# Optimization experiments

Measured on AMD Instinct MI355X. Metric: run time of the kernel, lower is better.

Reference implementation:

```python
import jax, jax.numpy as jnp
import numpy as np

B, T = 256, 64
ACT, EMB = 6, 1024
S, D = 32, 32          # stoch, discrete
SF = S * D             # flattened stochastic state (1024)
DET, HID = 600, 600


def _st_sample(logit, g):
    """Gumbel-max categorical sample with straight-through gradient.
    logit, g: [B, S, D]. Returns one-hot sample [B, S, D]."""
    idx = jnp.argmax(logit + g, axis=-1)
    onehot = jax.nn.one_hot(idx, logit.shape[-1], dtype=logit.dtype)
    probs = jax.nn.softmax(logit, axis=-1)
    return onehot + probs - jax.lax.stop_gradient(probs)


def setup_inputs() -> dict:
    key = jax.random.key(0)
    ks = jax.random.split(key, 20)
    p = lambda k, shp: (jax.random.normal(k, shp, dtype=jnp.float32) * 0.02)
    inp = {
        "action": jax.random.normal(ks[0], (B, T, ACT), dtype=jnp.float32),
        "embed": jax.random.normal(ks[1], (B, T, EMB), dtype=jnp.float32),
        "noise_img": jax.random.gumbel(ks[2], (B, T, S, D), dtype=jnp.float32),
        "noise_obs": jax.random.gumbel(ks[3], (B, T, S, D), dtype=jnp.float32),
        # img1: Dense(hidden, elu) on concat([stoch, action])
        "W_img1": p(ks[4], (SF + ACT, HID)), "b_img1": jnp.zeros((HID,), jnp.float32),
        # keras GRUCell (reset_after=True): gate order z, r, h; two biases
        "Wx": p(ks[5], (HID, 3 * DET)), "Wh": p(ks[6], (DET, 3 * DET)),
        "b_in": jnp.zeros((3 * DET,), jnp.float32), "b_rec": jnp.zeros((3 * DET,), jnp.float32),
        # img2: Dense(hidden, elu); img5: Dense(stoch*discrete)
        "W_img2": p(ks[7], (DET, HID)), "b_img2": jnp.zeros((HID,), jnp.float32),
        "W_img5": p(ks[8], (HID, SF)), "b_img5": jnp.zeros((SF,), jnp.float32),
        # obs1: Dense(hidden, elu) on concat([deter, embed]); obs3: Dense(stoch*discrete)
        "W_obs1": p(ks[9], (DET + EMB, HID)), "b_obs1": jnp.zeros((HID,), jnp.float32),
        "W_obs3": p(ks[10], (HID, SF)), "b_obs3": jnp.zeros((SF,), jnp.float32),
    }
    return inp


def reference(action, embed, noise_img, noise_obs,
              W_img1, b_img1, Wx, Wh, b_in, b_rec,
              W_img2, b_img2, W_img5, b_img5,
              W_obs1, b_obs1, W_obs3, b_obs3):
    # initial state: zeros (RSSM.initial)
    stoch0 = jnp.zeros((B, SF), jnp.float32)
    deter0 = jnp.zeros((B, DET), jnp.float32)

    def step(carry, inp):
        stoch, deter = carry                       # [B,SF], [B,DET]
        a, e, g_img, g_obs = inp
        # ---- img_step (prior) ----
        x = jax.nn.elu(jnp.concatenate([stoch, a], -1) @ W_img1 + b_img1)  # [B,HID]
        gx = x @ Wx + b_in                         # [B,3*DET]
        gh = deter @ Wh + b_rec
        xz, xr, xh = jnp.split(gx, 3, -1)
        hz, hr, hh = jnp.split(gh, 3, -1)
        z = jax.nn.sigmoid(xz + hz)
        r = jax.nn.sigmoid(xr + hr)
        cand = jnp.tanh(xh + r * hh)
        deter_n = z * deter + (1.0 - z) * cand     # [B,DET]
        y = jax.nn.elu(deter_n @ W_img2 + b_img2)
        logit_prior = (y @ W_img5 + b_img5).reshape(B, S, D)
        stoch_prior = _st_sample(logit_prior, g_img).reshape(B, SF)
        # ---- obs_step (post) ----
        o = jax.nn.elu(jnp.concatenate([deter_n, e], -1) @ W_obs1 + b_obs1)
        logit_post = (o @ W_obs3 + b_obs3).reshape(B, S, D)
        stoch_post = _st_sample(logit_post, g_obs).reshape(B, SF)
        out = (logit_post.reshape(B, SF), stoch_post, deter_n,
               logit_prior.reshape(B, SF), stoch_prior)
        return (stoch_post, deter_n), out

    xs = (jnp.swapaxes(action, 0, 1), jnp.swapaxes(embed, 0, 1),
          jnp.swapaxes(noise_img, 0, 1), jnp.swapaxes(noise_obs, 0, 1))
    _, outs = jax.lax.scan(step, (stoch0, deter0), xs)
    # outs: each [T,B,*] -> [B,T,*]; concat post_logit|post_stoch|deter|prior_logit|prior_stoch
    out = jnp.concatenate([jnp.swapaxes(o, 0, 1) for o in outs], axis=-1)  # [B,T,4*SF+DET]
    return out
```

## Files before the change

### kernel.cpp

```cpp
#include <hip/hip_runtime.h>
#include <math.h>

namespace {

constexpr int B = 256, T = 64, ACTN = 6, EMB = 1024;
constexpr int S = 32, DD = 32, SFN = 1024;
constexpr int DET = 600, HID = 600;
constexpr int OUTF = 4 * SFN + DET;

__device__ __forceinline__ float elu1(float x) { return x > 0.f ? x : expm1f(x); }
__device__ __forceinline__ float sigm(float x) { return 1.f / (1.f + expf(-x)); }

__global__ void kWB(const float* __restrict__ Wx, const float* __restrict__ Wh,
                    float* __restrict__ WBm) {
    int k = blockIdx.x;
    const float* src = (k < 600) ? (Wx + (size_t)k * 1800) : (Wh + (size_t)(k - 600) * 1800);
    for (int j = threadIdx.x; j < 600; j += blockDim.x) {
        size_t o = ((size_t)j * 1200 + k) * 3;
        WBm[o + 0] = src[j];
        WBm[o + 1] = src[600 + j];
        WBm[o + 2] = src[1200 + j];
    }
}

__global__ void kWC(const float* __restrict__ W2, const float* __restrict__ Wo1,
                    float* __restrict__ WCm) {
    int k = blockIdx.x;
    for (int j = threadIdx.x; j < 1200; j += blockDim.x) {
        float v = (j < 600) ? W2[(size_t)k * 600 + j] : Wo1[(size_t)k * 600 + (j - 600)];
        WCm[(size_t)j * 600 + k] = v;
    }
}

__global__ void kWD(const float* __restrict__ W5, const float* __restrict__ Wo3,
                    float* __restrict__ WDm) {
    int k = blockIdx.x;
    for (int j = threadIdx.x; j < 2048; j += blockDim.x) {
        float v = (j < 1024) ? W5[(size_t)k * 1024 + j] : Wo3[(size_t)k * 1024 + (j - 1024)];
        WDm[(size_t)j * 600 + k] = v;
    }
}

__global__ __launch_bounds__(512) void kPemb(const float* __restrict__ embed,
                                             const float* __restrict__ Wo1,
                                             const float* __restrict__ bo1,
                                             float* __restrict__ embPre) {
    int bid = blockIdx.x;
    int jg = bid % 10;
    int r = bid / 10;
    int bg = r & 3;
    int t = r >> 2;
    int tid = threadIdx.x;
    int lane = tid & 63;
    int wid = __builtin_amdgcn_readfirstlane(tid >> 6);
    int b0 = bg * 64;
    int j0 = jg * 64 + wid * 8;
    bool active = (j0 < 600);
    __shared__ float tile[64 * 129];
    float acc[8] = {0, 0, 0, 0, 0, 0, 0, 0};
    for (int kc = 0; kc < EMB; kc += 128) {
        __syncthreads();
        for (int ii = tid; ii < 64 * 128; ii += 512) {
            int i = ii >> 7, k = ii & 127;
            tile[i * 129 + k] = embed[((size_t)(b0 + i) * T + t) * EMB + kc + k];
        }
        __syncthreads();
        if (active) {
            const float* wbase = Wo1 + (size_t)(600 + kc) * 600 + j0;
#pragma unroll 4
            for (int k = 0; k < 128; ++k) {
                float v = tile[lane * 129 + k];
                float4 wa = *(const float4*)(wbase + (size_t)k * 600);
                float4 wb = *(const float4*)(wbase + (size_t)k * 600 + 4);
                acc[0] += v * wa.x; acc[1] += v * wa.y; acc[2] += v * wa.z; acc[3] += v * wa.w;
                acc[4] += v * wb.x; acc[5] += v * wb.y; acc[6] += v * wb.z; acc[7] += v * wb.w;
            }
        }
    }
    if (active) {
#pragma unroll
        for (int c = 0; c < 8; ++c)
            embPre[((size_t)t * 600 + j0 + c) * B + b0 + lane] = acc[c] + bo1[j0 + c];
    }
}

__global__ __launch_bounds__(256) void kA(const float* __restrict__ act,
                                          const float* __restrict__ W1,
                                          const float* __restrict__ b1,
                                          const int* __restrict__ idxB,
                                          float* __restrict__ xT, int t, int first) {
    int b = blockIdx.x, tid = threadIdx.x;
    __shared__ float sa[ACTN];
    __shared__ int si[S];
    if (tid < ACTN) sa[tid] = act[((size_t)b * T + t) * ACTN + tid];
    if (!first && tid < S) si[tid] = idxB[b * S + tid];
    __syncthreads();
    for (int h = tid; h < HID; h += 256) {
        float a = b1[h];
#pragma unroll
        for (int k = 0; k < ACTN; ++k) a += sa[k] * W1[(size_t)(SFN + k) * HID + h];
        if (!first) {
#pragma unroll 8
            for (int s = 0; s < S; ++s) a += W1[(size_t)(s * DD + si[s]) * HID + h];
        }
        xT[(size_t)h * B + b] = elu1(a);
    }
}

__global__ __launch_bounds__(512) void kB(const float* __restrict__ xT,
                                          const float* __restrict__ dPrev,
                                          const float* __restrict__ WBm,
                                          const float* __restrict__ b_in,
                                          const float* __restrict__ b_rec,
                                          float* __restrict__ dNext,
                                          float* __restrict__ out, int t) {
    int tid = threadIdx.x, lane = tid & 63;
    int wid = __builtin_amdgcn_readfirstlane(tid >> 6);
    int rg = blockIdx.x & 3, jg = blockIdx.x >> 2;
    int j = jg * 8 + wid;
    int b = rg * 64 + lane;
    const float* w = WBm + (size_t)j * 3600;
    float az = 0, ar = 0, ax = 0, ah = 0;
#pragma unroll 2
    for (int k = 0; k < 600; k += 4) {
        float4 wa = *(const float4*)(w + 3 * k);
        float4 wb = *(const float4*)(w + 3 * k + 4);
        float4 wc = *(const float4*)(w + 3 * k + 8);
        float x0 = xT[(size_t)(k + 0) * B + b];
        float x1 = xT[(size_t)(k + 1) * B + b];
        float x2 = xT[(size_t)(k + 2) * B + b];
        float x3 = xT[(size_t)(k + 3) * B + b];
        az += x0 * wa.x + x1 * wa.w + x2 * wb.z + x3 * wc.y;
        ar += x0 * wa.y + x1 * wb.x + x2 * wb.w + x3 * wc.z;
        ax += x0 * wa.z + x1 * wb.y + x2 * wc.x + x3 * wc.w;
    }
    const float* w2 = w + 1800;
#pragma unroll 2
    for (int k = 0; k < 600; k += 4) {
        float4 wa = *(const float4*)(w2 + 3 * k);
        float4 wb = *(const float4*)(w2 + 3 * k + 4);
        float4 wc = *(const float4*)(w2 + 3 * k + 8);
        float x0 = dPrev[(size_t)(k + 0) * B + b];
        float x1 = dPrev[(size_t)(k + 1) * B + b];
        float x2 = dPrev[(size_t)(k + 2) * B + b];
        float x3 = dPrev[(size_t)(k + 3) * B + b];
        az += x0 * wa.x + x1 * wa.w + x2 * wb.z + x3 * wc.y;
        ar += x0 * wa.y + x1 * wb.x + x2 * wb.w + x3 * wc.z;
        ah += x0 * wa.z + x1 * wb.y + x2 * wc.x + x3 * wc.w;
    }
    float dp = dPrev[(size_t)j * B + b];
    float z = sigm(az + b_in[j] + b_rec[j]);
    float rr = sigm(ar + b_in[600 + j] + b_rec[600 + j]);
    float cand = tanhf(ax + b_in[1200 + j] + rr * (ah + b_rec[1200 + j]));
    float dn = z * dp + (1.f - z) * cand;
    dNext[(size_t)j * B + b] = dn;
    out[((size_t)b * T + t) * OUTF + 2 * SFN + j] = dn;
}

__global__ __launch_bounds__(512) void kC(const float* __restrict__ dT,
                                          const float* __restrict__ WCm,
                                          const float* __restrict__ b2,
                                          const float* __restrict__ embPre,
                                          float* __restrict__ yoT, int t) {
    int tid = threadIdx.x, lane = tid & 63;
    int wid = __builtin_amdgcn_readfirstlane(tid >> 6);
    int rg = blockIdx.x & 3, jg = blockIdx.x >> 2;
    int j0 = jg * 16 + wid * 2;
    int b = rg * 64 + lane;
    const float* w0 = WCm + (size_t)j0 * 600;
    const float* w1 = w0 + 600;
    float a0 = 0, a1 = 0;
#pragma unroll 2
    for (int k = 0; k < 600; k += 4) {
        float4 p = *(const float4*)(w0 + k);
        float4 q = *(const float4*)(w1 + k);
        float v0 = dT[(size_t)(k + 0) * B + b];
        float v1 = dT[(size_t)(k + 1) * B + b];
        float v2 = dT[(size_t)(k + 2) * B + b];
        float v3 = dT[(size_t)(k + 3) * B + b];
        a0 += v0 * p.x + v1 * p.y + v2 * p.z + v3 * p.w;
        a1 += v0 * q.x + v1 * q.y + v2 * q.z + v3 * q.w;
    }
    if (j0 < 600) {
        yoT[(size_t)j0 * B + b] = elu1(a0 + b2[j0]);
        yoT[(size_t)(j0 + 1) * B + b] = elu1(a1 + b2[j0 + 1]);
    } else {
        int je = j0 - 600;
        yoT[(size_t)j0 * B + b] = elu1(a0 + embPre[((size_t)t * 600 + je) * B + b]);
        yoT[(size_t)(j0 + 1) * B + b] = elu1(a1 + embPre[((size_t)t * 600 + je + 1) * B + b]);
    }
}

__global__ __launch_bounds__(512) void kD(const float* __restrict__ yoT,
                                          const float* __restrict__ WDm,
                                          const float* __restrict__ b5,
                                          const float* __restrict__ bo3,
                                          const float* __restrict__ gImg,
                                          const float* __restrict__ gObs,
                                          float* __restrict__ out,
                                          int* __restrict__ idxB, int t) {
    int tid = threadIdx.x, lane = tid & 63;
    int wid = __builtin_amdgcn_readfirstlane(tid >> 6);
    int rg = blockIdx.x & 3, sg = blockIdx.x >> 2;
    int post = (sg >= 32) ? 1 : 0;
    int s = post ? sg - 32 : sg;
    int b = rg * 64 + lane;
    int dloc = wid * 4;
    int jglob = post * SFN + s * DD + dloc;
    const float* src = yoT + (post ? (size_t)600 * B : 0);
    const float* w0 = WDm + (size_t)jglob * 600;
    const float* w1 = w0 + 600;
    const float* w2 = w0 + 1200;
    const float* w3 = w0 + 1800;
    float a0 = 0, a1 = 0, a2 = 0, a3 = 0;
#pragma unroll 2
    for (int k = 0; k < 600; k += 4) {
        float4 p0 = *(const float4*)(w0 + k);
        float4 p1 = *(const float4*)(w1 + k);
        float4 p2 = *(const float4*)(w2 + k);
        float4 p3 = *(const float4*)(w3 + k);
        float v0 = src[(size_t)(k + 0) * B + b];
        float v1 = src[(size_t)(k + 1) * B + b];
        float v2 = src[(size_t)(k + 2) * B + b];
        float v3 = src[(size_t)(k + 3) * B + b];
        a0 += v0 * p0.x + v1 * p0.y + v2 * p0.z + v3 * p0.w;
        a1 += v0 * p1.x + v1 * p1.y + v2 * p1.z + v3 * p1.w;
        a2 += v0 * p2.x + v1 * p2.y + v2 * p2.z + v3 * p2.w;
        a3 += v0 * p3.x + v1 * p3.y + v2 * p3.z + v3 * p3.w;
    }
    const float* bias = post ? (bo3 + s * DD) : (b5 + s * DD);
    const float* g = (post ? gObs : gImg) + ((size_t)b * T + t) * SFN + s * DD;
    size_t obase = ((size_t)b * T + t) * OUTF;
    size_t lbase = obase + (post ? 0 : (2 * SFN + DET)) + s * DD;
    float vals[4];
    float accs[4] = {a0, a1, a2, a3};
#pragma unroll
    for (int c = 0; c < 4; ++c) {
        float lg = accs[c] + bias[dloc + c];
        out[lbase + dloc + c] = lg;
        vals[c] = lg + g[dloc + c];
    }
    float bm = vals[0];
    int bi = dloc;
#pragma unroll
    for (int c = 1; c < 4; ++c)
        if (vals[c] > bm) { bm = vals[c]; bi = dloc + c; }
    __shared__ float sm[8 * 64];
    __shared__ int sx[8 * 64];
    sm[wid * 64 + lane] = bm;
    sx[wid * 64 + lane] = bi;
    __syncthreads();
    float best = sm[lane];
    int bd = sx[lane];
#pragma unroll
    for (int w = 1; w < 8; ++w) {
        float v = sm[w * 64 + lane];
        if (v > best) { best = v; bd = sx[w * 64 + lane]; }
    }
    size_t sbase = obase + (post ? SFN : (3 * SFN + DET)) + s * DD;
#pragma unroll
    for (int c = 0; c < 4; ++c)
        out[sbase + dloc + c] = (dloc + c == bd) ? 1.f : 0.f;
    if (post && wid == 0) idxB[b * S + s] = bd;
}

}

extern "C" void kernel_launch(void* const* d_in, const int* in_sizes, int n_in,
                              void* d_out, int out_size, void* d_ws, size_t ws_size,
                              hipStream_t stream) {
    const float* action = (const float*)d_in[0];
    const float* embed  = (const float*)d_in[1];
    const float* gImg   = (const float*)d_in[2];
    const float* gObs   = (const float*)d_in[3];
    const float* W1     = (const float*)d_in[4];
    const float* b1     = (const float*)d_in[5];
    const float* Wx     = (const float*)d_in[6];
    const float* Wh     = (const float*)d_in[7];
    const float* b_in   = (const float*)d_in[8];
    const float* b_rec  = (const float*)d_in[9];
    const float* W2     = (const float*)d_in[10];
    const float* b2     = (const float*)d_in[11];
    const float* W5     = (const float*)d_in[12];
    const float* b5     = (const float*)d_in[13];
    const float* Wo1    = (const float*)d_in[14];
    const float* bo1    = (const float*)d_in[15];
    const float* Wo3    = (const float*)d_in[16];
    const float* bo3    = (const float*)d_in[17];
    float* out = (float*)d_out;

    float* ws = (float*)d_ws;
    float* WBm    = ws;
    float* WCm    = WBm + 2160000;
    float* WDm    = WCm + 720000;
    float* embPre = WDm + 1228800;
    float* xT     = embPre + 9830400;
    float* dA     = xT + 153600;
    float* dB     = dA + 153600;
    float* yoT    = dB + 153600;
    int*   idxB   = (int*)(yoT + 307200);

    hipMemsetAsync(dA, 0, 153600 * sizeof(float), stream);
    kWB<<<1200, 256, 0, stream>>>(Wx, Wh, WBm);
    kWC<<<600, 256, 0, stream>>>(W2, Wo1, WCm);
    kWD<<<600, 256, 0, stream>>>(W5, Wo3, WDm);
    kPemb<<<2560, 512, 0, stream>>>(embed, Wo1, bo1, embPre);

    for (int t = 0; t < T; ++t) {
        float* dP = (t & 1) ? dB : dA;
        float* dN = (t & 1) ? dA : dB;
        kA<<<256, 256, 0, stream>>>(action, W1, b1, idxB, xT, t, t == 0 ? 1 : 0);
        kB<<<300, 512, 0, stream>>>(xT, dP, WBm, b_in, b_rec, dN, out, t);
        kC<<<300, 512, 0, stream>>>(dN, WCm, b2, embPre, yoT, t);
        kD<<<256, 512, 0, stream>>>(yoT, WDm, b5, bo3, gImg, gObs, out, idxB, t);
    }
}
```

Baseline: 10.57 ms.

## Retile recurrent GEMV kernels so each wavefront covers 16 batches × 4 outputs

The GRU, hidden-dense and logit kernels are remapped so a 64-lane wavefront covers 16 batch rows by 4 output columns instead of 64 batch rows by one column. Weight rows are split per gate into separate planes. The categorical argmax in kD is now done with cross-lane shuffles instead of shared memory and a barrier. The goal is more weight reuse per load, lane-varying weight addresses, and more blocks for kC and kD. The cost is partly uncoalesced weight loads across the four column groups and different register pressure.

```diff
diff --git a/kernel.cpp b/kernel.cpp
--- a/kernel.cpp
+++ b/kernel.cpp
@@ -12,14 +12,12 @@
 __device__ __forceinline__ float sigm(float x) { return 1.f / (1.f + expf(-x)); }
 
 __global__ void kWB(const float* __restrict__ Wx, const float* __restrict__ Wh,
-                    float* __restrict__ WBm) {
+                    float* __restrict__ WBg) {
     int k = blockIdx.x;
     const float* src = (k < 600) ? (Wx + (size_t)k * 1800) : (Wh + (size_t)(k - 600) * 1800);
-    for (int j = threadIdx.x; j < 600; j += blockDim.x) {
-        size_t o = ((size_t)j * 1200 + k) * 3;
-        WBm[o + 0] = src[j];
-        WBm[o + 1] = src[600 + j];
-        WBm[o + 2] = src[1200 + j];
+    for (int i = threadIdx.x; i < 1800; i += blockDim.x) {
+        int g = i / 600, j = i % 600;
+        WBg[(size_t)g * 720000 + (size_t)j * 1200 + k] = src[i];
     }
 }
 
@@ -107,91 +105,118 @@
     }
 }
 
-__global__ __launch_bounds__(512) void kB(const float* __restrict__ xT,
+__global__ __launch_bounds__(256) void kB(const float* __restrict__ xT,
                                           const float* __restrict__ dPrev,
-                                          const float* __restrict__ WBm,
+                                          const float* __restrict__ WBg,
                                           const float* __restrict__ b_in,
                                           const float* __restrict__ b_rec,
                                           float* __restrict__ dNext,
                                           float* __restrict__ out, int t) {
-    int tid = threadIdx.x, lane = tid & 63;
-    int wid = __builtin_amdgcn_readfirstlane(tid >> 6);
-    int rg = blockIdx.x & 3, jg = blockIdx.x >> 2;
-    int j = jg * 8 + wid;
-    int b = rg * 64 + lane;
-    const float* w = WBm + (size_t)j * 3600;
-    float az = 0, ar = 0, ax = 0, ah = 0;
+    int tid = threadIdx.x, lane = tid & 63, wv = tid >> 6;
+    int bl = lane & 15, jl = lane >> 4;
+    int jg = blockIdx.x >> 2;
+    int bg = (blockIdx.x & 3) * 4 + wv;
+    int b = bg * 16 + bl;
+    int j0 = jg * 8 + jl;
+    const float* wz = WBg + (size_t)j0 * 1200;
+    const float* wr = wz + 720000;
+    const float* wc = wz + 1440000;
+    const float* xa = xT + b;
+    const float* da = dPrev + b;
+    float az0 = 0, ar0 = 0, ax0 = 0, ah0 = 0;
+    float az1 = 0, ar1 = 0, ax1 = 0, ah1 = 0;
 #pragma unroll 2
     for (int k = 0; k < 600; k += 4) {
-        float4 wa = *(const float4*)(w + 3 * k);
-        float4 wb = *(const float4*)(w + 3 * k + 4);
-        float4 wc = *(const float4*)(w + 3 * k + 8);
-        float x0 = xT[(size_t)(k + 0) * B + b];
-        float x1 = xT[(size_t)(k + 1) * B + b];
-        float x2 = xT[(size_t)(k + 2) * B + b];
-        float x3 = xT[(size_t)(k + 3) * B + b];
-        az += x0 * wa.x + x1 * wa.w + x2 * wb.z + x3 * wc.y;
-        ar += x0 * wa.y + x1 * wb.x + x2 * wb.w + x3 * wc.z;
-        ax += x0 * wa.z + x1 * wb.y + x2 * wc.x + x3 * wc.w;
-    }
-    const float* w2 = w + 1800;
+        float x0 = xa[(size_t)(k + 0) * B];
+        float x1 = xa[(size_t)(k + 1) * B];
+        float x2 = xa[(size_t)(k + 2) * B];
+        float x3 = xa[(size_t)(k + 3) * B];
+        float4 z0 = *(const float4*)(wz + k), z1 = *(const float4*)(wz + 4800 + k);
+        float4 r0 = *(const float4*)(wr + k), r1 = *(const float4*)(wr + 4800 + k);
+        float4 c0 = *(const float4*)(wc + k), c1 = *(const float4*)(wc + 4800 + k);
+        az0 += x0 * z0.x + x1 * z0.y + x2 * z0.z + x3 * z0.w;
+        az1 += x0 * z1.x + x1 * z1.y + x2 * z1.z + x3 * z1.w;
+        ar0 += x0 * r0.x + x1 * r0.y + x2 * r0.z + x3 * r0.w;
+        ar1 += x0 * r1.x + x1 * r1.y + x2 * r1.z + x3 * r1.w;
+        ax0 += x0 * c0.x + x1 * c0.y + x2 * c0.z + x3 * c0.w;
+        ax1 += x0 * c1.x + x1 * c1.y + x2 * c1.z + x3 * c1.w;
+    }
 #pragma unroll 2
     for (int k = 0; k < 600; k += 4) {
-        float4 wa = *(const float4*)(w2 + 3 * k);
-        float4 wb = *(const float4*)(w2 + 3 * k + 4);
-        float4 wc = *(const float4*)(w2 + 3 * k + 8);
-        float x0 = dPrev[(size_t)(k + 0) * B + b];
-        float x1 = dPrev[(size_t)(k + 1) * B + b];
-        float x2 = dPrev[(size_t)(k + 2) * B + b];
-        float x3 = dPrev[(size_t)(k + 3) * B + b];
-        az += x0 * wa.x + x1 * wa.w + x2 * wb.z + x3 * wc.y;
-        ar += x0 * wa.y + x1 * wb.x + x2 * wb.w + x3 * wc.z;
-        ah += x0 * wa.z + x1 * wb.y + x2 * wc.x + x3 * wc.w;
-    }
-    float dp = dPrev[(size_t)j * B + b];
-    float z = sigm(az + b_in[j] + b_rec[j]);
-    float rr = sigm(ar + b_in[600 + j] + b_rec[600 + j]);
-    float cand = tanhf(ax + b_in[1200 + j] + rr * (ah + b_rec[1200 + j]));
-    float dn = z * dp + (1.f - z) * cand;
-    dNext[(size_t)j * B + b] = dn;
-    out[((size_t)b * T + t) * OUTF + 2 * SFN + j] = dn;
-}
-
-__global__ __launch_bounds__(512) void kC(const float* __restrict__ dT,
+        float x0 = da[(size_t)(k + 0) * B];
+        float x1 = da[(size_t)(k + 1) * B];
+        float x2 = da[(size_t)(k + 2) * B];
+        float x3 = da[(size_t)(k + 3) * B];
+        float4 z0 = *(const float4*)(wz + 600 + k), z1 = *(const float4*)(wz + 5400 + k);
+        float4 r0 = *(const float4*)(wr + 600 + k), r1 = *(const float4*)(wr + 5400 + k);
+        float4 c0 = *(const float4*)(wc + 600 + k), c1 = *(const float4*)(wc + 5400 + k);
+        az0 += x0 * z0.x + x1 * z0.y + x2 * z0.z + x3 * z0.w;
+        az1 += x0 * z1.x + x1 * z1.y + x2 * z1.z + x3 * z1.w;
+        ar0 += x0 * r0.x + x1 * r0.y + x2 * r0.z + x3 * r0.w;
+        ar1 += x0 * r1.x + x1 * r1.y + x2 * r1.z + x3 * r1.w;
+        ah0 += x0 * c0.x + x1 * c0.y + x2 * c0.z + x3 * c0.w;
+        ah1 += x0 * c1.x + x1 * c1.y + x2 * c1.z + x3 * c1.w;
+    }
+    size_t ob = ((size_t)b * T + t) * OUTF + 2 * SFN;
+    {
+        int j = j0;
+        float dp = dPrev[(size_t)j * B + b];
+        float z = sigm(az0 + b_in[j] + b_rec[j]);
+        float rr = sigm(ar0 + b_in[600 + j] + b_rec[600 + j]);
+        float cd = tanhf(ax0 + b_in[1200 + j] + rr * (ah0 + b_rec[1200 + j]));
+        float dn = z * dp + (1.f - z) * cd;
+        dNext[(size_t)j * B + b] = dn;
+        out[ob + j] = dn;
+    }
+    {
+        int j = j0 + 4;
+        float dp = dPrev[(size_t)j * B + b];
+        float z = sigm(az1 + b_in[j] + b_rec[j]);
+        float rr = sigm(ar1 + b_in[600 + j] + b_rec[600 + j]);
+        float cd = tanhf(ax1 + b_in[1200 + j] + rr * (ah1 + b_rec[1200 + j]));
+        float dn = z * dp + (1.f - z) * cd;
+        dNext[(size_t)j * B + b] = dn;
+        out[ob + j] = dn;
+    }
+}
+
+__global__ __launch_bounds__(256) void kC(const float* __restrict__ dT,
                                           const float* __restrict__ WCm,
                                           const float* __restrict__ b2,
                                           const float* __restrict__ embPre,
                                           float* __restrict__ yoT, int t) {
-    int tid = threadIdx.x, lane = tid & 63;
-    int wid = __builtin_amdgcn_readfirstlane(tid >> 6);
-    int rg = blockIdx.x & 3, jg = blockIdx.x >> 2;
-    int j0 = jg * 16 + wid * 2;
-    int b = rg * 64 + lane;
+    int tid = threadIdx.x, lane = tid & 63, wv = tid >> 6;
+    int bl = lane & 15, jl = lane >> 4;
+    int jg = blockIdx.x >> 2;
+    int bg = (blockIdx.x & 3) * 4 + wv;
+    int b = bg * 16 + bl;
+    int j0 = jg * 8 + jl;
     const float* w0 = WCm + (size_t)j0 * 600;
-    const float* w1 = w0 + 600;
+    const float* w1 = w0 + 2400;
+    const float* da = dT + b;
     float a0 = 0, a1 = 0;
 #pragma unroll 2
     for (int k = 0; k < 600; k += 4) {
+        float x0 = da[(size_t)(k + 0) * B];
+        float x1 = da[(size_t)(k + 1) * B];
+        float x2 = da[(size_t)(k + 2) * B];
+        float x3 = da[(size_t)(k + 3) * B];
         float4 p = *(const float4*)(w0 + k);
         float4 q = *(const float4*)(w1 + k);
-        float v0 = dT[(size_t)(k + 0) * B + b];
-        float v1 = dT[(size_t)(k + 1) * B + b];
-        float v2 = dT[(size_t)(k + 2) * B + b];
-        float v3 = dT[(size_t)(k + 3) * B + b];
-        a0 += v0 * p.x + v1 * p.y + v2 * p.z + v3 * p.w;
-        a1 += v0 * q.x + v1 * q.y + v2 * q.z + v3 * q.w;
-    }
-    if (j0 < 600) {
-        yoT[(size_t)j0 * B + b] = elu1(a0 + b2[j0]);
-        yoT[(size_t)(j0 + 1) * B + b] = elu1(a1 + b2[j0 + 1]);
-    } else {
-        int je = j0 - 600;
-        yoT[(size_t)j0 * B + b] = elu1(a0 + embPre[((size_t)t * 600 + je) * B + b]);
-        yoT[(size_t)(j0 + 1) * B + b] = elu1(a1 + embPre[((size_t)t * 600 + je + 1) * B + b]);
-    }
-}
-
-__global__ __launch_bounds__(512) void kD(const float* __restrict__ yoT,
+        a0 += x0 * p.x + x1 * p.y + x2 * p.z + x3 * p.w;
+        a1 += x0 * q.x + x1 * q.y + x2 * q.z + x3 * q.w;
+    }
+#pragma unroll
+    for (int ja = 0; ja < 2; ++ja) {
+        int j = j0 + 4 * ja;
+        float a = ja ? a1 : a0;
+        float v = (j < 600) ? elu1(a + b2[j])
+                            : elu1(a + embPre[((size_t)t * 600 + (j - 600)) * B + b]);
+        yoT[(size_t)j * B + b] = v;
+    }
+}
+
+__global__ __launch_bounds__(128) void kD(const float* __restrict__ yoT,
                                           const float* __restrict__ WDm,
                                           const float* __restrict__ b5,
                                           const float* __restrict__ bo3,
@@ -199,69 +224,51 @@
                                           const float* __restrict__ gObs,
                                           float* __restrict__ out,
                                           int* __restrict__ idxB, int t) {
-    int tid = threadIdx.x, lane = tid & 63;
-    int wid = __builtin_amdgcn_readfirstlane(tid >> 6);
-    int rg = blockIdx.x & 3, sg = blockIdx.x >> 2;
+    int tid = threadIdx.x, lane = tid & 63, wv = tid >> 6;
+    int bl = lane & 15, jl = lane >> 4;
+    int sg = blockIdx.x >> 3;
+    int bg = (blockIdx.x & 7) * 2 + wv;
     int post = (sg >= 32) ? 1 : 0;
     int s = post ? sg - 32 : sg;
-    int b = rg * 64 + lane;
-    int dloc = wid * 4;
-    int jglob = post * SFN + s * DD + dloc;
-    const float* src = yoT + (post ? (size_t)600 * B : 0);
-    const float* w0 = WDm + (size_t)jglob * 600;
-    const float* w1 = w0 + 600;
-    const float* w2 = w0 + 1200;
-    const float* w3 = w0 + 1800;
-    float a0 = 0, a1 = 0, a2 = 0, a3 = 0;
+    int b = bg * 16 + bl;
+    const float* src = yoT + (post ? (size_t)600 * B : 0) + b;
+    const float* w = WDm + ((size_t)(post * SFN) + s * DD + jl) * 600;
+    float acc[8] = {0, 0, 0, 0, 0, 0, 0, 0};
 #pragma unroll 2
     for (int k = 0; k < 600; k += 4) {
-        float4 p0 = *(const float4*)(w0 + k);
-        float4 p1 = *(const float4*)(w1 + k);
-        float4 p2 = *(const float4*)(w2 + k);
-        float4 p3 = *(const float4*)(w3 + k);
-        float v0 = src[(size_t)(k + 0) * B + b];
-        float v1 = src[(size_t)(k + 1) * B + b];
-        float v2 = src[(size_t)(k + 2) * B + b];
-        float v3 = src[(size_t)(k + 3) * B + b];
-        a0 += v0 * p0.x + v1 * p0.y + v2 * p0.z + v3 * p0.w;
-        a1 += v0 * p1.x + v1 * p1.y + v2 * p1.z + v3 * p1.w;
-        a2 += v0 * p2.x + v1 * p2.y + v2 * p2.z + v3 * p2.w;
-        a3 += v0 * p3.x + v1 * p3.y + v2 * p3.z + v3 * p3.w;
-    }
-    const float* bias = post ? (bo3 + s * DD) : (b5 + s * DD);
-    const float* g = (post ? gObs : gImg) + ((size_t)b * T + t) * SFN + s * DD;
+        float x0 = src[(size_t)(k + 0) * B];
+        float x1 = src[(size_t)(k + 1) * B];
+        float x2 = src[(size_t)(k + 2) * B];
+        float x3 = src[(size_t)(k + 3) * B];
+#pragma unroll
+        for (int ja = 0; ja < 8; ++ja) {
+            float4 p = *(const float4*)(w + (size_t)ja * 2400 + k);
+            acc[ja] += x0 * p.x + x1 * p.y + x2 * p.z + x3 * p.w;
+        }
+    }
+    const float* bias = (post ? bo3 : b5) + s * DD + jl;
+    const float* g = (post ? gObs : gImg) + ((size_t)b * T + t) * SFN + s * DD + jl;
     size_t obase = ((size_t)b * T + t) * OUTF;
-    size_t lbase = obase + (post ? 0 : (2 * SFN + DET)) + s * DD;
-    float vals[4];
-    float accs[4] = {a0, a1, a2, a3};
-#pragma unroll
-    for (int c = 0; c < 4; ++c) {
-        float lg = accs[c] + bias[dloc + c];
-        out[lbase + dloc + c] = lg;
-        vals[c] = lg + g[dloc + c];
-    }
-    float bm = vals[0];
-    int bi = dloc;
-#pragma unroll
-    for (int c = 1; c < 4; ++c)
-        if (vals[c] > bm) { bm = vals[c]; bi = dloc + c; }
-    __shared__ float sm[8 * 64];
-    __shared__ int sx[8 * 64];
-    sm[wid * 64 + lane] = bm;
-    sx[wid * 64 + lane] = bi;
-    __syncthreads();
-    float best = sm[lane];
-    int bd = sx[lane];
-#pragma unroll
-    for (int w = 1; w < 8; ++w) {
-        float v = sm[w * 64 + lane];
-        if (v > best) { best = v; bd = sx[w * 64 + lane]; }
-    }
-    size_t sbase = obase + (post ? SFN : (3 * SFN + DET)) + s * DD;
-#pragma unroll
-    for (int c = 0; c < 4; ++c)
-        out[sbase + dloc + c] = (dloc + c == bd) ? 1.f : 0.f;
-    if (post && wid == 0) idxB[b * S + s] = bd;
+    size_t lbase = obase + (post ? 0 : 2 * SFN + DET) + s * DD + jl;
+    size_t sbase = obase + (post ? SFN : 3 * SFN + DET) + s * DD + jl;
+    float bm = -INFINITY;
+    int bi = 0;
+#pragma unroll
+    for (int ja = 0; ja < 8; ++ja) {
+        float lg = acc[ja] + bias[ja * 4];
+        out[lbase + ja * 4] = lg;
+        float v = lg + g[ja * 4];
+        if (v > bm) { bm = v; bi = ja * 4 + jl; }
+    }
+    for (int m = 16; m < 64; m <<= 1) {
+        float ov = __shfl_xor(bm, m, 64);
+        int oi = __shfl_xor(bi, m, 64);
+        if (ov > bm || (ov == bm && oi < bi)) { bm = ov; bi = oi; }
+    }
+#pragma unroll
+    for (int ja = 0; ja < 8; ++ja)
+        out[sbase + ja * 4] = (ja * 4 + jl == bi) ? 1.f : 0.f;
+    if (post && jl == 0) idxB[b * S + s] = bi;
 }
 
 }
@@ -290,8 +297,8 @@
     float* out = (float*)d_out;
 
     float* ws = (float*)d_ws;
-    float* WBm    = ws;
-    float* WCm    = WBm + 2160000;
+    float* WBg    = ws;
+    float* WCm    = WBg + 2160000;
     float* WDm    = WCm + 720000;
     float* embPre = WDm + 1228800;
     float* xT     = embPre + 9830400;
@@ -301,7 +308,7 @@
     int*   idxB   = (int*)(yoT + 307200);
 
     hipMemsetAsync(dA, 0, 153600 * sizeof(float), stream);
-    kWB<<<1200, 256, 0, stream>>>(Wx, Wh, WBm);
+    kWB<<<1200, 256, 0, stream>>>(Wx, Wh, WBg);
     kWC<<<600, 256, 0, stream>>>(W2, Wo1, WCm);
     kWD<<<600, 256, 0, stream>>>(W5, Wo3, WDm);
     kPemb<<<2560, 512, 0, stream>>>(embed, Wo1, bo1, embPre);
@@ -310,8 +317,8 @@
         float* dP = (t & 1) ? dB : dA;
         float* dN = (t & 1) ? dA : dB;
         kA<<<256, 256, 0, stream>>>(action, W1, b1, idxB, xT, t, t == 0 ? 1 : 0);
-        kB<<<300, 512, 0, stream>>>(xT, dP, WBm, b_in, b_rec, dN, out, t);
-        kC<<<300, 512, 0, stream>>>(dN, WCm, b2, embPre, yoT, t);
-        kD<<<256, 512, 0, stream>>>(yoT, WDm, b5, bo3, gImg, gObs, out, idxB, t);
-    }
-}
+        kB<<<300, 256, 0, stream>>>(xT, dP, WBg, b_in, b_rec, dN, out, t);
+        kC<<<600, 256, 0, stream>>>(dN, WCm, b2, embPre, yoT, t);
+        kD<<<512, 128, 0, stream>>>(yoT, WDm, b5, bo3, gImg, gObs, out, idxB, t);
+    }
+}
```

After: 14.76 ms. 1.4x slower.
